# Performance work log

Measured on AMD Instinct MI355X. Metric: run time of the kernel, lower is better.

The kernel has to match this reference:

```python
import jax, jax.numpy as jnp
import numpy as np

H, DQ, DK, DV, DM = 16, 64, 64, 64, 1024
NEG = -1.0e12


def setup_inputs() -> dict:
    key = jax.random.key(0)
    ks = jax.random.split(key, 16)
    B, S = 4, 1024
    s = 0.02
    inp = {
        "query": jax.random.normal(ks[0], (B, S, DM), jnp.float32),
        "key": jax.random.normal(ks[1], (B, S, DM), jnp.float32),
        "value": jax.random.normal(ks[2], (B, S, DM), jnp.float32),
        "mask": jax.random.randint(ks[3], (B, S), 0, 2, jnp.int32),
        "Wq": jax.random.normal(ks[4], (H * DQ, DM), jnp.float32) * s,
        "bq": jnp.zeros((H * DQ,), jnp.float32),
        "Wk": jax.random.normal(ks[5], (H * DK, DM), jnp.float32) * s,
        "bk": jnp.zeros((H * DK,), jnp.float32),
        "Wv": jax.random.normal(ks[6], (H * DV, DM), jnp.float32) * s,
        "bv": jnp.zeros((H * DV,), jnp.float32),
        "Wo": jax.random.normal(ks[7], (DM, H * DV), jnp.float32) * s,
        "bo": jnp.zeros((DM,), jnp.float32),
        "ln_g": jnp.ones((DM,), jnp.float32),
        "ln_b": jnp.zeros((DM,), jnp.float32),
    }
    return inp


def _attention(query, key, value, mask, Wq, bq, Wk, bk, Wv, bv, Wo, bo, ln_g, ln_b):
    B, qL, _ = query.shape
    kL = key.shape[1]
    mf = mask.astype(jnp.float32)  # [B, kL] ; 1 = masked token
    # padding mask broadcast over query rows, then self-attn: masked query rows fully masked
    m = jnp.broadcast_to(mf[:, None, :], (B, qL, kL))
    m = jnp.where(mf[:, :, None] > 0, 1.0, m)  # [B, q, k]

    def proj(x, W, b, d):
        # [B,S,DM] -> [H,B,S,d]
        return (x @ W.T + b).reshape(B, -1, H, d).transpose(2, 0, 1, 3)

    q = proj(query, Wq, bq, DQ)
    k = proj(key, Wk, bk, DK)
    v = proj(value, Wv, bv, DV)

    scores = jnp.einsum("hbqd,hbkd->hbqk", q, k) / np.float32(np.sqrt(DK))
    fut = jnp.triu(jnp.ones((qL, kL), jnp.float32), k=1)  # [q,k] future mask
    scores = scores + m[None] * NEG + fut[None, None] * NEG
    attn = jax.nn.softmax(scores, axis=-1)
    attn = attn * (1.0 - m[None]) * (1.0 - fut[None, None])

    out = jnp.einsum("hbqk,hbkd->hbqd", attn, v)  # [H,B,q,DV]
    out = out.transpose(1, 2, 0, 3).reshape(B, qL, H * DV)
    out = out @ Wo.T + bo + query  # residual
    mu = jnp.mean(out, axis=-1, keepdims=True)
    var = jnp.mean(jnp.square(out - mu), axis=-1, keepdims=True)
    out = (out - mu) * jax.lax.rsqrt(var + 1e-12) * ln_g + ln_b
    return out, attn.reshape(H * B, qL, kL)


def reference(query, key, value, mask, Wq, bq, Wk, bk, Wv, bv, Wo, bo, ln_g, ln_b):
    return _attention(query, key, value, mask, Wq, bq, Wk, bk, Wv, bv, Wo, bo, ln_g, ln_b)
```

## Files before the change

### kernel.cpp

```cpp
#include <hip/hip_runtime.h>
#include <hip/hip_bf16.h>

typedef __attribute__((ext_vector_type(4))) float f32x4;
typedef __attribute__((ext_vector_type(4))) float fv4;
typedef __attribute__((ext_vector_type(8))) short bf16x8;
typedef __attribute__((ext_vector_type(4))) short bf16x4;

#define DEVI __device__ __forceinline__

constexpr int BATCH = 4, SEQ = 1024, NH = 16, HD = 64, DM_ = 1024;
constexpr int NTOK = BATCH * SEQ;

DEVI unsigned short f2bf(float f) {
  union { float f; unsigned u; } v; v.f = f;
  unsigned r = v.u + 0x7FFFu + ((v.u >> 16) & 1u);
  return (unsigned short)(r >> 16);
}

DEVI int swz64(int row, int col) {
  int byte = (row * 64 + col) * 2;
  byte ^= (row & 7) << 4;
  return byte >> 1;
}

DEVI void gld_lds16(const unsigned short* g, unsigned short* l) {
  __builtin_amdgcn_global_load_lds(
      (const __attribute__((address_space(1))) unsigned int*)g,
      (__attribute__((address_space(3))) unsigned int*)l, 16, 0, 0);
}

__global__ __launch_bounds__(256) void k_cvt(
    const float* __restrict__ q, const float* __restrict__ k,
    const float* __restrict__ v,
    const float* __restrict__ wq, const float* __restrict__ wk,
    const float* __restrict__ wv, const float* __restrict__ wo,
    unsigned short* __restrict__ Xb, unsigned short* __restrict__ Wb)
{
  const int a = blockIdx.y;
  const float* src;
  unsigned short* dst;
  int n;
  if (a < 3) {
    src = (a == 0) ? q : (a == 1) ? k : v;
    dst = Xb + (size_t)a * NTOK * DM_;
    n = NTOK * DM_;
  } else {
    src = (a == 3) ? wq : (a == 4) ? wk : (a == 5) ? wv : wo;
    dst = Wb + (size_t)(a - 3) * DM_ * DM_;
    n = DM_ * DM_;
  }
  const int idx = (blockIdx.x * 256 + threadIdx.x) * 8;
  if (idx >= n) return;
  fv4 v0 = *(const fv4*)(src + idx);
  fv4 v1 = *(const fv4*)(src + idx + 4);
  bf16x8 o;
  o[0] = (short)f2bf(v0[0]); o[1] = (short)f2bf(v0[1]);
  o[2] = (short)f2bf(v0[2]); o[3] = (short)f2bf(v0[3]);
  o[4] = (short)f2bf(v1[0]); o[5] = (short)f2bf(v1[1]);
  o[6] = (short)f2bf(v1[2]); o[7] = (short)f2bf(v1[3]);
  *(bf16x8*)(dst + idx) = o;
}

__global__ __launch_bounds__(256) void k_proj(
    const unsigned short* __restrict__ Xb, const unsigned short* __restrict__ Wb,
    const float* __restrict__ bq, const float* __restrict__ bk,
    const float* __restrict__ bv,
    unsigned short* __restrict__ qo, unsigned short* __restrict__ ko,
    unsigned short* __restrict__ vTo)
{
  const int z = blockIdx.z;
  const unsigned short* X = Xb + (size_t)z * NTOK * DM_;
  const unsigned short* W = Wb + (size_t)z * DM_ * DM_;
  const float* bias = (z == 0) ? bq : (z == 1) ? bk : bv;

  __shared__ __align__(16) unsigned short Al[128 * 64];
  __shared__ __align__(16) unsigned short Bl[128 * 64];

  const int tid = threadIdx.x;
  const int lane = tid & 63;
  const int w = tid >> 6;
  const int wm = w & 1, wn = w >> 1;
  const int l15 = lane & 15, lg = lane >> 4;
  const int m0 = blockIdx.x * 128;
  const int o0 = blockIdx.y * 128;

  const int rseg = lane >> 3;
  const int cg = (lane & 7) ^ rseg;

  f32x4 acc[4][4];
#pragma unroll
  for (int i = 0; i < 4; ++i)
#pragma unroll
    for (int j = 0; j < 4; ++j) acc[i][j] = f32x4{0.f, 0.f, 0.f, 0.f};

  for (int kt = 0; kt < 16; ++kt) {
    const int k0 = kt * 64;
    __syncthreads();
#pragma unroll
    for (int i = 0; i < 4; ++i) {
      const int seg = w * 4 + i;
      const int row = seg * 8 + rseg;
      gld_lds16(X + (size_t)(m0 + row) * DM_ + k0 + cg * 8, &Al[seg * 512]);
      gld_lds16(W + (size_t)(o0 + row) * DM_ + k0 + cg * 8, &Bl[seg * 512]);
    }
    __syncthreads();
#pragma unroll
    for (int kk = 0; kk < 2; ++kk) {
      bf16x8 af[4], bfm[4];
#pragma unroll
      for (int m = 0; m < 4; ++m)
        af[m] = *(const bf16x8*)&Al[swz64(wm * 64 + m * 16 + l15, kk * 32 + lg * 8)];
#pragma unroll
      for (int n = 0; n < 4; ++n)
        bfm[n] = *(const bf16x8*)&Bl[swz64(wn * 64 + n * 16 + l15, kk * 32 + lg * 8)];
#pragma unroll
      for (int m = 0; m < 4; ++m)
#pragma unroll
        for (int n = 0; n < 4; ++n)
          acc[m][n] = __builtin_amdgcn_mfma_f32_16x16x32_bf16(af[m], bfm[n], acc[m][n], 0, 0, 0);
    }
  }

#pragma unroll
  for (int n = 0; n < 4; ++n) {
    const int oc = o0 + wn * 64 + n * 16 + l15;
    const float bb = bias[oc];
#pragma unroll
    for (int m = 0; m < 4; ++m) {
      const int rbase = m0 + wm * 64 + m * 16 + lg * 4;
      if (z == 2) {
        bf16x4 pv;
#pragma unroll
        for (int j = 0; j < 4; ++j) pv[j] = (short)f2bf(acc[m][n][j] + bb);
        *(bf16x4*)&vTo[((size_t)(rbase >> 10) * 1024 + oc) * 1024 + (rbase & 1023)] = pv;
      } else {
        unsigned short* Y = (z == 0) ? qo : ko;
        const float sc = (z == 0) ? 0.125f : 1.f;
#pragma unroll
        for (int j = 0; j < 4; ++j)
          Y[(size_t)(rbase + j) * DM_ + oc] = f2bf((acc[m][n][j] + bb) * sc);
      }
    }
  }
}

__global__ __launch_bounds__(256) void k_attn_pv(
    const unsigned short* __restrict__ qb, const unsigned short* __restrict__ kb,
    const unsigned short* __restrict__ vT, const int* __restrict__ mask,
    float* __restrict__ attn, unsigned short* __restrict__ Ob)
{
  const int tid = threadIdx.x;
  const int lane = tid & 63;
  const int w = tid >> 6;
  const int l15 = lane & 15, lg = lane >> 4;
  const int hb = blockIdx.y;
  const int h = hb >> 2, b = hb & 3;
  const int t = blockIdx.x;
  const int q0 = t * 16;
  const int qglob = q0 + l15;

  __shared__ __align__(16) unsigned short Pl[16 * 1024];
  __shared__ float red[4][16];

  const unsigned short* qp = qb + (size_t)(b * SEQ + qglob) * DM_ + h * HD + lg * 8;
  const bf16x8 qf0 = *(const bf16x8*)qp;
  const bf16x8 qf1 = *(const bf16x8*)(qp + 32);

  const int qm = mask[b * SEQ + qglob];
  const int ni = (t >= w) ? (((t - w) >> 2) + 1) : 0;

  f32x4 acc[16];
#pragma unroll
  for (int i = 0; i < 16; ++i) acc[i] = f32x4{0.f, 0.f, 0.f, 0.f};

#pragma unroll
  for (int i = 0; i < 16; ++i) {
    if (i < ni) {
      const int krow = (w + 4 * i) * 16 + l15;
      const unsigned short* kp = kb + (size_t)(b * SEQ + krow) * DM_ + h * HD + lg * 8;
      bf16x8 kf0 = *(const bf16x8*)kp;
      bf16x8 kf1 = *(const bf16x8*)(kp + 32);
      acc[i] = __builtin_amdgcn_mfma_f32_16x16x32_bf16(kf0, qf0, acc[i], 0, 0, 0);
      acc[i] = __builtin_amdgcn_mfma_f32_16x16x32_bf16(kf1, qf1, acc[i], 0, 0, 0);
    }
  }

  unsigned long long kv = 0;
#pragma unroll
  for (int i = 0; i < 16; ++i) {
    if (i < ni) {
      const int kbase = (w + 4 * i) * 16 + lg * 4;
      int4 mv = *(const int4*)&mask[b * SEQ + kbase];
      if (mv.x == 0) kv |= 1ull << (i * 4 + 0);
      if (mv.y == 0) kv |= 1ull << (i * 4 + 1);
      if (mv.z == 0) kv |= 1ull << (i * 4 + 2);
      if (mv.w == 0) kv |= 1ull << (i * 4 + 3);
    }
  }
  if (qm != 0) kv = 0;

  float m = -1e30f;
#pragma unroll
  for (int i = 0; i < 16; ++i) {
    if (i < ni) {
      const int kbase = (w + 4 * i) * 16 + lg * 4;
#pragma unroll
      for (int j = 0; j < 4; ++j)
        if (((kv >> (i * 4 + j)) & 1ull) && (kbase + j <= qglob))
          m = fmaxf(m, acc[i][j]);
    }
  }
  m = fmaxf(m, __shfl_xor(m, 16, 64));
  m = fmaxf(m, __shfl_xor(m, 32, 64));
  if (lane < 16) red[w][l15] = m;
  __syncthreads();
  m = fmaxf(fmaxf(red[0][l15], red[1][l15]), fmaxf(red[2][l15], red[3][l15]));
  __syncthreads();

  float s = 0.f;
#pragma unroll
  for (int i = 0; i < 16; ++i) {
    if (i < ni) {
      const int kbase = (w + 4 * i) * 16 + lg * 4;
#pragma unroll
      for (int j = 0; j < 4; ++j) {
        const bool vld = ((kv >> (i * 4 + j)) & 1ull) && (kbase + j <= qglob);
        const float p = vld ? __expf(acc[i][j] - m) : 0.f;
        acc[i][j] = p;
        s += p;
      }
    }
  }
  s += __shfl_xor(s, 16, 64);
  s += __shfl_xor(s, 32, 64);
  if (lane < 16) red[w][l15] = s;
  __syncthreads();
  s = red[0][l15] + red[1][l15] + red[2][l15] + red[3][l15];
  const float rinv = (s > 0.f) ? (1.f / s) : 0.f;

  float* ap = attn + (size_t)hb * SEQ * SEQ + (size_t)qglob * SEQ;
#pragma unroll
  for (int i = 0; i < 16; ++i) {
    const int kbase = (w + 4 * i) * 16 + lg * 4;
    const int pbyte = ((l15 * 1024 + kbase) * 2) ^ ((l15 & 7) << 4);
    if (i < ni) {
      fv4 st;
      bf16x4 pb;
#pragma unroll
      for (int j = 0; j < 4; ++j) {
        st[j] = acc[i][j] * rinv;
        pb[j] = (short)f2bf(acc[i][j]);
      }
      *(fv4*)&ap[kbase] = st;
      *(bf16x4*)((char*)Pl + pbyte) = pb;
    } else {
      *(fv4*)&ap[kbase] = fv4{0.f, 0.f, 0.f, 0.f};
      *(bf16x4*)((char*)Pl + pbyte) = bf16x4{0, 0, 0, 0};
    }
  }
  __syncthreads();

  const int kt_lim = (q0 >> 5) + 1;
  f32x4 o = f32x4{0.f, 0.f, 0.f, 0.f};
  const unsigned short* vp = vT + (size_t)(b * 1024 + h * HD + w * 16 + l15) * 1024;
#pragma unroll 4
  for (int kt = 0; kt < kt_lim; ++kt) {
    const int k0 = kt * 32 + lg * 8;
    bf16x8 vf = *(const bf16x8*)(vp + k0);
    const int pbyte = ((l15 * 1024 + k0) * 2) ^ ((l15 & 7) << 4);
    bf16x8 pf = *(const bf16x8*)((const char*)Pl + pbyte);
    o = __builtin_amdgcn_mfma_f32_16x16x32_bf16(vf, pf, o, 0, 0, 0);
  }

  bf16x4 ob;
#pragma unroll
  for (int j = 0; j < 4; ++j) ob[j] = (short)f2bf(o[j] * rinv);
  *(bf16x4*)&Ob[(size_t)(b * SEQ + qglob) * DM_ + h * HD + w * 16 + lg * 4] = ob;
}

__global__ __launch_bounds__(256) void k_oproj(
    const unsigned short* __restrict__ Ob, const unsigned short* __restrict__ Wb,
    const float* __restrict__ bo, const float* __restrict__ query,
    float* __restrict__ preln)
{
  const unsigned short* W = Wb + (size_t)3 * DM_ * DM_;

  __shared__ __align__(16) unsigned short Al[128 * 64];
  __shared__ __align__(16) unsigned short Bl[128 * 64];

  const int tid = threadIdx.x;
  const int lane = tid & 63;
  const int w = tid >> 6;
  const int wm = w & 1, wn = w >> 1;
  const int l15 = lane & 15, lg = lane >> 4;
  const int m0 = blockIdx.x * 128;
  const int o0 = blockIdx.y * 128;

  const int rseg = lane >> 3;
  const int cg = (lane & 7) ^ rseg;

  f32x4 acc[4][4];
#pragma unroll
  for (int i = 0; i < 4; ++i)
#pragma unroll
    for (int j = 0; j < 4; ++j) acc[i][j] = f32x4{0.f, 0.f, 0.f, 0.f};

  for (int kt = 0; kt < 16; ++kt) {
    const int k0 = kt * 64;
    __syncthreads();
#pragma unroll
    for (int i = 0; i < 4; ++i) {
      const int seg = w * 4 + i;
      const int row = seg * 8 + rseg;
      gld_lds16(Ob + (size_t)(m0 + row) * DM_ + k0 + cg * 8, &Al[seg * 512]);
      gld_lds16(W + (size_t)(o0 + row) * DM_ + k0 + cg * 8, &Bl[seg * 512]);
    }
    __syncthreads();
#pragma unroll
    for (int kk = 0; kk < 2; ++kk) {
      bf16x8 af[4], bfm[4];
#pragma unroll
      for (int m = 0; m < 4; ++m)
        af[m] = *(const bf16x8*)&Al[swz64(wm * 64 + m * 16 + l15, kk * 32 + lg * 8)];
#pragma unroll
      for (int n = 0; n < 4; ++n)
        bfm[n] = *(const bf16x8*)&Bl[swz64(wn * 64 + n * 16 + l15, kk * 32 + lg * 8)];
#pragma unroll
      for (int m = 0; m < 4; ++m)
#pragma unroll
        for (int n = 0; n < 4; ++n)
          acc[m][n] = __builtin_amdgcn_mfma_f32_16x16x32_bf16(af[m], bfm[n], acc[m][n], 0, 0, 0);
    }
  }

#pragma unroll
  for (int n = 0; n < 4; ++n) {
    const int oc = o0 + wn * 64 + n * 16 + l15;
    const float bb = bo[oc];
#pragma unroll
    for (int m = 0; m < 4; ++m) {
      const int rbase = m0 + wm * 64 + m * 16 + lg * 4;
#pragma unroll
      for (int j = 0; j < 4; ++j) {
        const size_t idx = (size_t)(rbase + j) * DM_ + oc;
        preln[idx] = acc[m][n][j] + bb + query[idx];
      }
    }
  }
}

__global__ __launch_bounds__(256) void k_ln(
    const float* __restrict__ x, const float* __restrict__ g,
    const float* __restrict__ bta, float* __restrict__ out)
{
  const int row = blockIdx.x;
  const int tid = threadIdx.x;
  const float* xr = x + (size_t)row * DM_;
  fv4 v = *(const fv4*)(xr + tid * 4);
  float s = v[0] + v[1] + v[2] + v[3];
  float s2 = v[0] * v[0] + v[1] * v[1] + v[2] * v[2] + v[3] * v[3];
#pragma unroll
  for (int off = 1; off < 64; off <<= 1) {
    s += __shfl_xor(s, off, 64);
    s2 += __shfl_xor(s2, off, 64);
  }
  __shared__ float rs[2][4];
  const int w = tid >> 6;
  if ((tid & 63) == 0) { rs[0][w] = s; rs[1][w] = s2; }
  __syncthreads();
  s = rs[0][0] + rs[0][1] + rs[0][2] + rs[0][3];
  s2 = rs[1][0] + rs[1][1] + rs[1][2] + rs[1][3];
  const float mu = s * (1.f / 1024.f);
  const float var = s2 * (1.f / 1024.f) - mu * mu;
  const float rstd = rsqrtf(var + 1e-12f);
  fv4 gg = *(const fv4*)(g + tid * 4);
  fv4 bb = *(const fv4*)(bta + tid * 4);
  fv4 o;
#pragma unroll
  for (int j = 0; j < 4; ++j) o[j] = (v[j] - mu) * rstd * gg[j] + bb[j];
  *(fv4*)(out + (size_t)row * DM_ + tid * 4) = o;
}

extern "C" void kernel_launch(void* const* d_in, const int* in_sizes, int n_in,
                              void* d_out, int out_size, void* d_ws, size_t ws_size,
                              hipStream_t stream) {
  const float* query = (const float*)d_in[0];
  const float* key   = (const float*)d_in[1];
  const float* value = (const float*)d_in[2];
  const int*   mask  = (const int*)d_in[3];
  const float* Wq = (const float*)d_in[4];
  const float* bq = (const float*)d_in[5];
  const float* Wk = (const float*)d_in[6];
  const float* bk = (const float*)d_in[7];
  const float* Wv = (const float*)d_in[8];
  const float* bv = (const float*)d_in[9];
  const float* Wo = (const float*)d_in[10];
  const float* bo = (const float*)d_in[11];
  const float* ln_g = (const float*)d_in[12];
  const float* ln_b = (const float*)d_in[13];

  float* out  = (float*)d_out;
  float* attn = out + (size_t)NTOK * DM_;

  char* ws = (char*)d_ws;
  unsigned short* Xb = (unsigned short*)ws;
  unsigned short* Wb = Xb + (size_t)3 * NTOK * DM_;
  unsigned short* qb = Wb + (size_t)4 * DM_ * DM_;
  unsigned short* kb = qb + (size_t)NTOK * DM_;
  unsigned short* vT = kb + (size_t)NTOK * DM_;
  unsigned short* Ob = vT + (size_t)NTOK * DM_;
  float* preln = (float*)ws;

  k_cvt<<<dim3(2048, 7), 256, 0, stream>>>(query, key, value, Wq, Wk, Wv, Wo,
                                           Xb, Wb);
  k_proj<<<dim3(32, 8, 3), 256, 0, stream>>>(Xb, Wb, bq, bk, bv, qb, kb, vT);
  k_attn_pv<<<dim3(64, 64), 256, 0, stream>>>(qb, kb, vT, mask, attn, Ob);
  k_oproj<<<dim3(32, 8), 256, 0, stream>>>(Ob, Wb, bo, query, preln);
  k_ln<<<4096, 256, 0, stream>>>(preln, ln_g, ln_b, out);
}
```

Baseline: 526.4 us.

## Halve GEMM M-tiles and compute PV directly from score registers without LDS staging

```diff
diff --git a/kernel.cpp b/kernel.cpp
--- a/kernel.cpp
+++ b/kernel.cpp
@@ -73,7 +73,7 @@
   const unsigned short* W = Wb + (size_t)z * DM_ * DM_;
   const float* bias = (z == 0) ? bq : (z == 1) ? bk : bv;
 
-  __shared__ __align__(16) unsigned short Al[128 * 64];
+  __shared__ __align__(16) unsigned short Al[64 * 64];
   __shared__ __align__(16) unsigned short Bl[128 * 64];
 
   const int tid = threadIdx.x;
@@ -81,15 +81,15 @@
   const int w = tid >> 6;
   const int wm = w & 1, wn = w >> 1;
   const int l15 = lane & 15, lg = lane >> 4;
-  const int m0 = blockIdx.x * 128;
+  const int m0 = blockIdx.x * 64;
   const int o0 = blockIdx.y * 128;
 
   const int rseg = lane >> 3;
   const int cg = (lane & 7) ^ rseg;
 
-  f32x4 acc[4][4];
-#pragma unroll
-  for (int i = 0; i < 4; ++i)
+  f32x4 acc[2][4];
+#pragma unroll
+  for (int i = 0; i < 2; ++i)
 #pragma unroll
     for (int j = 0; j < 4; ++j) acc[i][j] = f32x4{0.f, 0.f, 0.f, 0.f};
 
@@ -97,24 +97,27 @@
     const int k0 = kt * 64;
     __syncthreads();
 #pragma unroll
+    for (int i = 0; i < 2; ++i) {
+      const int seg = w * 2 + i;
+      gld_lds16(X + (size_t)(m0 + seg * 8 + rseg) * DM_ + k0 + cg * 8, &Al[seg * 512]);
+    }
+#pragma unroll
     for (int i = 0; i < 4; ++i) {
       const int seg = w * 4 + i;
-      const int row = seg * 8 + rseg;
-      gld_lds16(X + (size_t)(m0 + row) * DM_ + k0 + cg * 8, &Al[seg * 512]);
-      gld_lds16(W + (size_t)(o0 + row) * DM_ + k0 + cg * 8, &Bl[seg * 512]);
+      gld_lds16(W + (size_t)(o0 + seg * 8 + rseg) * DM_ + k0 + cg * 8, &Bl[seg * 512]);
     }
     __syncthreads();
 #pragma unroll
     for (int kk = 0; kk < 2; ++kk) {
-      bf16x8 af[4], bfm[4];
-#pragma unroll
-      for (int m = 0; m < 4; ++m)
-        af[m] = *(const bf16x8*)&Al[swz64(wm * 64 + m * 16 + l15, kk * 32 + lg * 8)];
+      bf16x8 af[2], bfm[4];
+#pragma unroll
+      for (int m = 0; m < 2; ++m)
+        af[m] = *(const bf16x8*)&Al[swz64(wm * 32 + m * 16 + l15, kk * 32 + lg * 8)];
 #pragma unroll
       for (int n = 0; n < 4; ++n)
         bfm[n] = *(const bf16x8*)&Bl[swz64(wn * 64 + n * 16 + l15, kk * 32 + lg * 8)];
 #pragma unroll
-      for (int m = 0; m < 4; ++m)
+      for (int m = 0; m < 2; ++m)
 #pragma unroll
         for (int n = 0; n < 4; ++n)
           acc[m][n] = __builtin_amdgcn_mfma_f32_16x16x32_bf16(af[m], bfm[n], acc[m][n], 0, 0, 0);
@@ -126,8 +129,8 @@
     const int oc = o0 + wn * 64 + n * 16 + l15;
     const float bb = bias[oc];
 #pragma unroll
-    for (int m = 0; m < 4; ++m) {
-      const int rbase = m0 + wm * 64 + m * 16 + lg * 4;
+    for (int m = 0; m < 2; ++m) {
+      const int rbase = m0 + wm * 32 + m * 16 + lg * 4;
       if (z == 2) {
         bf16x4 pv;
 #pragma unroll
@@ -159,8 +162,9 @@
   const int q0 = t * 16;
   const int qglob = q0 + l15;
 
-  __shared__ __align__(16) unsigned short Pl[16 * 1024];
+  __shared__ float Ow[4][64 * 18];
   __shared__ float red[4][16];
+  __shared__ float ssum[16];
 
   const unsigned short* qp = qb + (size_t)(b * SEQ + qglob) * DM_ + h * HD + lg * 8;
   const bf16x8 qf0 = *(const bf16x8*)qp;
@@ -236,46 +240,71 @@
   if (lane < 16) red[w][l15] = s;
   __syncthreads();
   s = red[0][l15] + red[1][l15] + red[2][l15] + red[3][l15];
+  if (w == 0 && lane < 16) ssum[l15] = s;
   const float rinv = (s > 0.f) ? (1.f / s) : 0.f;
 
   float* ap = attn + (size_t)hb * SEQ * SEQ + (size_t)qglob * SEQ;
 #pragma unroll
   for (int i = 0; i < 16; ++i) {
     const int kbase = (w + 4 * i) * 16 + lg * 4;
-    const int pbyte = ((l15 * 1024 + kbase) * 2) ^ ((l15 & 7) << 4);
+    fv4 st = fv4{0.f, 0.f, 0.f, 0.f};
     if (i < ni) {
-      fv4 st;
-      bf16x4 pb;
-#pragma unroll
-      for (int j = 0; j < 4; ++j) {
-        st[j] = acc[i][j] * rinv;
-        pb[j] = (short)f2bf(acc[i][j]);
+#pragma unroll
+      for (int j = 0; j < 4; ++j) st[j] = acc[i][j] * rinv;
+    }
+    *(fv4*)&ap[kbase] = st;
+  }
+
+  f32x4 o[4];
+#pragma unroll
+  for (int dt = 0; dt < 4; ++dt) o[dt] = f32x4{0.f, 0.f, 0.f, 0.f};
+  const int nc = (ni + 1) >> 1;
+  const unsigned short* vbase = vT + (size_t)(b * 1024 + h * HD) * 1024;
+#pragma unroll
+  for (int c = 0; c < 8; ++c) {
+    if (c < nc) {
+      const bool hasB = (2 * c + 1 < ni);
+      bf16x8 pb;
+#pragma unroll
+      for (int j = 0; j < 4; ++j) pb[j] = (short)f2bf(acc[2 * c][j]);
+#pragma unroll
+      for (int j = 0; j < 4; ++j)
+        pb[4 + j] = hasB ? (short)f2bf(acc[2 * c + 1][j]) : (short)0;
+      const int kA = (w + 8 * c) * 16 + lg * 4;
+      const int kB = hasB ? kA + 64 : kA;
+#pragma unroll
+      for (int dt = 0; dt < 4; ++dt) {
+        const unsigned short* vr = vbase + (size_t)(dt * 16 + l15) * 1024;
+        bf16x4 a0 = *(const bf16x4*)(vr + kA);
+        bf16x4 a1 = *(const bf16x4*)(vr + kB);
+        bf16x8 af;
+        af[0] = a0[0]; af[1] = a0[1]; af[2] = a0[2]; af[3] = a0[3];
+        af[4] = a1[0]; af[5] = a1[1]; af[6] = a1[2]; af[7] = a1[3];
+        o[dt] = __builtin_amdgcn_mfma_f32_16x16x32_bf16(af, pb, o[dt], 0, 0, 0);
       }
-      *(fv4*)&ap[kbase] = st;
-      *(bf16x4*)((char*)Pl + pbyte) = pb;
-    } else {
-      *(fv4*)&ap[kbase] = fv4{0.f, 0.f, 0.f, 0.f};
-      *(bf16x4*)((char*)Pl + pbyte) = bf16x4{0, 0, 0, 0};
-    }
-  }
+    }
+  }
+
+#pragma unroll
+  for (int dt = 0; dt < 4; ++dt)
+#pragma unroll
+    for (int j = 0; j < 4; ++j)
+      Ow[w][(dt * 16 + lg * 4 + j) * 18 + l15] = o[dt][j];
   __syncthreads();
 
-  const int kt_lim = (q0 >> 5) + 1;
-  f32x4 o = f32x4{0.f, 0.f, 0.f, 0.f};
-  const unsigned short* vp = vT + (size_t)(b * 1024 + h * HD + w * 16 + l15) * 1024;
-#pragma unroll 4
-  for (int kt = 0; kt < kt_lim; ++kt) {
-    const int k0 = kt * 32 + lg * 8;
-    bf16x8 vf = *(const bf16x8*)(vp + k0);
-    const int pbyte = ((l15 * 1024 + k0) * 2) ^ ((l15 & 7) << 4);
-    bf16x8 pf = *(const bf16x8*)((const char*)Pl + pbyte);
-    o = __builtin_amdgcn_mfma_f32_16x16x32_bf16(vf, pf, o, 0, 0, 0);
-  }
-
+  const int qr = tid >> 4;
+  const int d0 = (tid & 15) * 4;
+  const float sq = ssum[qr];
+  const float ri = (sq > 0.f) ? (1.f / sq) : 0.f;
   bf16x4 ob;
 #pragma unroll
-  for (int j = 0; j < 4; ++j) ob[j] = (short)f2bf(o[j] * rinv);
-  *(bf16x4*)&Ob[(size_t)(b * SEQ + qglob) * DM_ + h * HD + w * 16 + lg * 4] = ob;
+  for (int j = 0; j < 4; ++j) {
+    const int d = d0 + j;
+    const float v = Ow[0][d * 18 + qr] + Ow[1][d * 18 + qr] +
+                    Ow[2][d * 18 + qr] + Ow[3][d * 18 + qr];
+    ob[j] = (short)f2bf(v * ri);
+  }
+  *(bf16x4*)&Ob[(size_t)(b * SEQ + q0 + qr) * DM_ + h * HD + d0] = ob;
 }
 
 __global__ __launch_bounds__(256) void k_oproj(
@@ -285,7 +314,7 @@
 {
   const unsigned short* W = Wb + (size_t)3 * DM_ * DM_;
 
-  __shared__ __align__(16) unsigned short Al[128 * 64];
+  __shared__ __align__(16) unsigned short Al[64 * 64];
   __shared__ __align__(16) unsigned short Bl[128 * 64];
 
   const int tid = threadIdx.x;
@@ -293,15 +322,15 @@
   const int w = tid >> 6;
   const int wm = w & 1, wn = w >> 1;
   const int l15 = lane & 15, lg = lane >> 4;
-  const int m0 = blockIdx.x * 128;
+  const int m0 = blockIdx.x * 64;
   const int o0 = blockIdx.y * 128;
 
   const int rseg = lane >> 3;
   const int cg = (lane & 7) ^ rseg;
 
-  f32x4 acc[4][4];
-#pragma unroll
-  for (int i = 0; i < 4; ++i)
+  f32x4 acc[2][4];
+#pragma unroll
+  for (int i = 0; i < 2; ++i)
 #pragma unroll
     for (int j = 0; j < 4; ++j) acc[i][j] = f32x4{0.f, 0.f, 0.f, 0.f};
 
@@ -309,24 +338,27 @@
     const int k0 = kt * 64;
     __syncthreads();
 #pragma unroll
+    for (int i = 0; i < 2; ++i) {
+      const int seg = w * 2 + i;
+      gld_lds16(Ob + (size_t)(m0 + seg * 8 + rseg) * DM_ + k0 + cg * 8, &Al[seg * 512]);
+    }
+#pragma unroll
     for (int i = 0; i < 4; ++i) {
       const int seg = w * 4 + i;
-      const int row = seg * 8 + rseg;
-      gld_lds16(Ob + (size_t)(m0 + row) * DM_ + k0 + cg * 8, &Al[seg * 512]);
-      gld_lds16(W + (size_t)(o0 + row) * DM_ + k0 + cg * 8, &Bl[seg * 512]);
+      gld_lds16(W + (size_t)(o0 + seg * 8 + rseg) * DM_ + k0 + cg * 8, &Bl[seg * 512]);
     }
     __syncthreads();
 #pragma unroll
     for (int kk = 0; kk < 2; ++kk) {
-      bf16x8 af[4], bfm[4];
-#pragma unroll
-      for (int m = 0; m < 4; ++m)
-        af[m] = *(const bf16x8*)&Al[swz64(wm * 64 + m * 16 + l15, kk * 32 + lg * 8)];
+      bf16x8 af[2], bfm[4];
+#pragma unroll
+      for (int m = 0; m < 2; ++m)
+        af[m] = *(const bf16x8*)&Al[swz64(wm * 32 + m * 16 + l15, kk * 32 + lg * 8)];
 #pragma unroll
       for (int n = 0; n < 4; ++n)
         bfm[n] = *(const bf16x8*)&Bl[swz64(wn * 64 + n * 16 + l15, kk * 32 + lg * 8)];
 #pragma unroll
-      for (int m = 0; m < 4; ++m)
+      for (int m = 0; m < 2; ++m)
 #pragma unroll
         for (int n = 0; n < 4; ++n)
           acc[m][n] = __builtin_amdgcn_mfma_f32_16x16x32_bf16(af[m], bfm[n], acc[m][n], 0, 0, 0);
@@ -338,8 +370,8 @@
     const int oc = o0 + wn * 64 + n * 16 + l15;
     const float bb = bo[oc];
 #pragma unroll
-    for (int m = 0; m < 4; ++m) {
-      const int rbase = m0 + wm * 64 + m * 16 + lg * 4;
+    for (int m = 0; m < 2; ++m) {
+      const int rbase = m0 + wm * 32 + m * 16 + lg * 4;
 #pragma unroll
       for (int j = 0; j < 4; ++j) {
         const size_t idx = (size_t)(rbase + j) * DM_ + oc;
@@ -413,8 +445,8 @@
 
   k_cvt<<<dim3(2048, 7), 256, 0, stream>>>(query, key, value, Wq, Wk, Wv, Wo,
                                            Xb, Wb);
-  k_proj<<<dim3(32, 8, 3), 256, 0, stream>>>(Xb, Wb, bq, bk, bv, qb, kb, vT);
+  k_proj<<<dim3(64, 8, 3), 256, 0, stream>>>(Xb, Wb, bq, bk, bv, qb, kb, vT);
   k_attn_pv<<<dim3(64, 64), 256, 0, stream>>>(qb, kb, vT, mask, attn, Ob);
-  k_oproj<<<dim3(32, 8), 256, 0, stream>>>(Ob, Wb, bo, query, preln);
+  k_oproj<<<dim3(64, 8), 256, 0, stream>>>(Ob, Wb, bo, query, preln);
   k_ln<<<4096, 256, 0, stream>>>(preln, ln_g, ln_b, out);
 }
```

New measurement: 557.3 us. 1.06x slower.
